# Kernel optimization log

Measured on AMD Instinct MI355X. Metric: run time of the kernel, lower is better.

## Reference

```python
import jax, jax.numpy as jnp
import numpy as np

N_NODES = 50000
N_EDGES = 800000
N_FEAT = 128
N_HID = 128
N_CLASS = 40


def _mean_aggregate(x, src, dst, num_nodes):
    # PyG 'mean' aggregation: for each target node, mean of source-neighbor features.
    msgs = x[src]                                             # [E, D] gather
    sums = jax.ops.segment_sum(msgs, dst, num_segments=num_nodes)   # [N, D]
    ones = jnp.ones((src.shape[0],), dtype=x.dtype)
    cnt = jax.ops.segment_sum(ones, dst, num_segments=num_nodes)    # [N]
    return sums / jnp.maximum(cnt, 1.0)[:, None]


def setup_inputs() -> dict:
    key = jax.random.key(0)
    ks = jax.random.split(key, 8)
    x = jax.random.normal(ks[0], (N_NODES, N_FEAT), dtype=jnp.float32)
    edge_index = jax.random.randint(ks[1], (2, N_EDGES), 0, N_NODES, dtype=jnp.int64)
    s1 = 1.0 / np.sqrt(N_FEAT)
    s2 = 1.0 / np.sqrt(N_HID)
    return {
        "x": x,
        "edge_index": edge_index,
        # SAGEConv 1: lin_l acts on aggregated neighbors (has bias), lin_r on root (no bias)
        "Wl1": jax.random.normal(ks[2], (N_FEAT, N_HID), dtype=jnp.float32) * s1,
        "Wr1": jax.random.normal(ks[3], (N_FEAT, N_HID), dtype=jnp.float32) * s1,
        "b1": jnp.zeros((N_HID,), dtype=jnp.float32),
        # SAGEConv 2 (gc2)
        "Wl2": jax.random.normal(ks[4], (N_HID, N_CLASS), dtype=jnp.float32) * s2,
        "Wr2": jax.random.normal(ks[5], (N_HID, N_CLASS), dtype=jnp.float32) * s2,
        "b2": jnp.zeros((N_CLASS,), dtype=jnp.float32),
    }


def reference(x, edge_index, Wl1, Wr1, b1, Wl2, Wr2, b2):
    src, dst = edge_index[0], edge_index[1]
    n = x.shape[0]
    # Layer 1: SAGEConv -> relu (dropout is identity in eval mode)
    agg = _mean_aggregate(x, src, dst, n)                 # [N, F]
    h = jax.nn.relu(agg @ Wl1 + x @ Wr1 + b1)             # [N, H]
    # Layer 2: SAGEConv (logits)
    agg2 = _mean_aggregate(h, src, dst, n)                # [N, H]
    out = agg2 @ Wl2 + h @ Wr2 + b2                       # [N, C]
    return out
```

## Files before the change

kernel.cpp:

```cpp
#include <hip/hip_runtime.h>
#include <hip/hip_bf16.h>

#define N_FEAT 128
#define N_HID  128
#define N_CLASS 40

#define NP   256
#define PSZ  196
#define BCAP 4096
#define BCHUNK 4096

#define HSTRIDE 136

typedef __attribute__((ext_vector_type(8))) __bf16 bf16x8;
typedef __attribute__((ext_vector_type(4))) float f32x4;

__device__ __forceinline__ unsigned short f2bf(float f) {
    union { float f; unsigned int u; } v; v.f = f;
    unsigned int r = (v.u + 0x7FFFu + ((v.u >> 16) & 1u)) >> 16;
    return (unsigned short)r;
}
__device__ __forceinline__ float bf2f_lo(unsigned int p) {
    union { unsigned int u; float f; } v; v.u = p << 16; return v.f;
}
__device__ __forceinline__ float bf2f_hi(unsigned int p) {
    union { unsigned int u; float f; } v; v.u = p & 0xFFFF0000u; return v.f;
}

__device__ __forceinline__ void swz_body(const float* __restrict__ W,
                                         unsigned short* __restrict__ sw,
                                         int ncols, int t, int nt) {
    if (t >= nt * 4 * 64) return;
    int lane = t & 63;
    int bi = t >> 6;
    int kc = bi & 3, ct = bi >> 2;
    int n = lane & 15, q = lane >> 4;
    int col = ct * 16 + n;
    #pragma unroll
    for (int j = 0; j < 8; ++j) {
        int k = kc * 32 + q * 8 + j;
        float f = (col < ncols) ? W[(size_t)k * ncols + col] : 0.f;
        sw[(size_t)t * 8 + j] = f2bf(f);
    }
}
__device__ __forceinline__ void swzc_body(const float* __restrict__ Wl2,
                                          const float* __restrict__ Wr2,
                                          unsigned short* __restrict__ sw, int t) {
    if (t >= 5 * 4 * 64) return;
    int lane = t & 63;
    int bi = t >> 6;
    int kc = bi & 3, ct = bi >> 2;
    int n = lane & 15, q = lane >> 4;
    int col = ct * 16 + n;
    #pragma unroll
    for (int j = 0; j < 8; ++j) {
        int k = kc * 32 + q * 8 + j;
        float f = (col < N_CLASS) ? Wl2[(size_t)k * N_CLASS + col]
                                  : Wr2[(size_t)k * N_CLASS + (col - N_CLASS)];
        sw[(size_t)t * 8 + j] = f2bf(f);
    }
}

__global__ __launch_bounds__(256) void k_prep(const float* __restrict__ x,
                                              unsigned short* __restrict__ xb, int nCvt, int nElem,
                                              const float* __restrict__ Wl1,
                                              const float* __restrict__ Wr1,
                                              const float* __restrict__ Wl2,
                                              const float* __restrict__ Wr2,
                                              unsigned short* __restrict__ w1l,
                                              unsigned short* __restrict__ w1r,
                                              unsigned short* __restrict__ wc,
                                              int* __restrict__ ptail) {
    int b = blockIdx.x, t = threadIdx.x;
    if (b < nCvt) {
        int i = (b * 256 + t) * 4;
        if (i < nElem) {
            float4 v = *(const float4*)(x + i);
            ushort4 o;
            o.x = f2bf(v.x); o.y = f2bf(v.y); o.z = f2bf(v.z); o.w = f2bf(v.w);
            *(ushort4*)(xb + i) = o;
        }
        return;
    }
    b -= nCvt;
    if (b < 8) { swz_body(Wl1, w1l, N_HID, b * 256 + t, 8); return; }
    b -= 8;
    if (b < 8) { swz_body(Wr1, w1r, N_HID, b * 256 + t, 8); return; }
    b -= 8;
    if (b < 5) { swzc_body(Wl2, Wr2, wc, b * 256 + t); return; }
    ptail[t] = 0;
}

__global__ __launch_bounds__(256) void k_bin(const int* __restrict__ src,
                                             const int* __restrict__ dst,
                                             int* __restrict__ ptail,
                                             uint2* __restrict__ bins, int E) {
    __shared__ uint2 stage[BCHUNK];
    __shared__ int lcnt[NP], lofs[NP], lcur[NP], gbase[NP];
    __shared__ int ws4[4];
    int t = threadIdx.x;
    int base = blockIdx.x * BCHUNK;
    int nE = min(BCHUNK, E - base);
    lcnt[t] = 0;
    __syncthreads();
    for (int i = t; i < nE; i += 256) {
        int d = dst[base + i];
        atomicAdd(&lcnt[d / PSZ], 1);
    }
    __syncthreads();
    {
        int v = lcnt[t];
        int lane = t & 63, wid = t >> 6;
        int inc = v;
        #pragma unroll
        for (int s = 1; s < 64; s <<= 1) {
            int u = __shfl_up(inc, s);
            if (lane >= s) inc += u;
        }
        if (lane == 63) ws4[wid] = inc;
        __syncthreads();
        int wb = 0;
        for (int w = 0; w < wid; ++w) wb += ws4[w];
        int exc = wb + inc - v;
        lofs[t] = exc;
        lcur[t] = exc;
        gbase[t] = atomicAdd(&ptail[t], v);
    }
    __syncthreads();
    for (int i = t; i < nE; i += 256) {
        int d = dst[base + i];
        int s = src[base + i];
        int pos = atomicAdd(&lcur[d / PSZ], 1);
        stage[pos] = make_uint2((unsigned)s, (unsigned)d);
    }
    __syncthreads();
    for (int i = t; i < nE; i += 256) {
        uint2 pr = stage[i];
        int p = (int)pr.y / PSZ;
        bins[(size_t)p * BCAP + gbase[p] + (i - lofs[p])] = pr;
    }
}

__global__ __launch_bounds__(256) void k_build(const uint2* __restrict__ bins,
                                               const int* __restrict__ ptail,
                                               int* __restrict__ off,
                                               int* __restrict__ srt, int N) {
    int p = blockIdx.x;
    int t = threadIdx.x;
    __shared__ int ws4[4];
    __shared__ int sexc[NP];
    __shared__ int lc[256], lofs[256];
    {
        int v = ptail[t];
        int lane = t & 63, wid = t >> 6;
        int inc = v;
        #pragma unroll
        for (int s = 1; s < 64; s <<= 1) {
            int u = __shfl_up(inc, s);
            if (lane >= s) inc += u;
        }
        if (lane == 63) ws4[wid] = inc;
        __syncthreads();
        int wb = 0;
        for (int w = 0; w < wid; ++w) wb += ws4[w];
        sexc[t] = wb + inc - v;
        if (p == NP - 1 && t == NP - 1) off[N] = wb + inc;
    }
    lc[t] = 0;
    __syncthreads();
    int pb = sexc[p];
    int n = ptail[p];
    const uint2* bp = bins + (size_t)p * BCAP;
    for (int i = t; i < n; i += 256)
        atomicAdd(&lc[(int)bp[i].y - p * PSZ], 1);
    __syncthreads();
    {
        int v = lc[t];
        int lane = t & 63, wid = t >> 6;
        int inc = v;
        #pragma unroll
        for (int s = 1; s < 64; s <<= 1) {
            int u = __shfl_up(inc, s);
            if (lane >= s) inc += u;
        }
        if (lane == 63) ws4[wid] = inc;
        __syncthreads();
        int wb = 0;
        for (int w = 0; w < wid; ++w) wb += ws4[w];
        lofs[t] = pb + wb + inc - v;
    }
    __syncthreads();
    int g = p * PSZ + t;
    if (t < PSZ && g < N) off[g] = lofs[t];
    __syncthreads();
    for (int i = t; i < n; i += 256) {
        uint2 pr = bp[i];
        int pos = atomicAdd(&lofs[(int)pr.y - p * PSZ], 1);
        srt[pos] = (int)pr.x;
    }
}

__global__ __launch_bounds__(256) void k_aggb4(const unsigned short* __restrict__ feat,
                                               const int* __restrict__ srt,
                                               const int* __restrict__ off,
                                               unsigned short* __restrict__ outp, int n_nodes) {
    int wave = (blockIdx.x * blockDim.x + threadIdx.x) >> 6;
    int lane = threadIdx.x & 63;
    if (wave >= n_nodes) return;
    int q = lane >> 4;
    int l = lane & 15;
    int beg = off[wave];
    int end = off[wave + 1];
    float a0 = 0.f, a1 = 0.f, a2 = 0.f, a3 = 0.f,
          a4 = 0.f, a5 = 0.f, a6 = 0.f, a7 = 0.f;
    int e = beg + q;
    #define ACCUM128(P) { \
        a0 += bf2f_lo(P.x); a1 += bf2f_hi(P.x); \
        a2 += bf2f_lo(P.y); a3 += bf2f_hi(P.y); \
        a4 += bf2f_lo(P.z); a5 += bf2f_hi(P.z); \
        a6 += bf2f_lo(P.w); a7 += bf2f_hi(P.w); }
    for (; e + 4 < end; e += 8) {
        int s0 = srt[e];
        int s1 = srt[e + 4];
        uint4 p0 = *(const uint4*)(feat + (size_t)s0 * N_FEAT + l * 8);
        uint4 p1 = *(const uint4*)(feat + (size_t)s1 * N_FEAT + l * 8);
        ACCUM128(p0)
        ACCUM128(p1)
    }
    if (e < end) {
        int s0 = srt[e];
        uint4 p0 = *(const uint4*)(feat + (size_t)s0 * N_FEAT + l * 8);
        ACCUM128(p0)
    }
    #undef ACCUM128
    #define RED(A) A += __shfl_xor(A, 16); A += __shfl_xor(A, 32);
    RED(a0) RED(a1) RED(a2) RED(a3) RED(a4) RED(a5) RED(a6) RED(a7)
    #undef RED
    if (q == 0) {
        int c = end - beg;
        float inv = 1.0f / (float)(c > 1 ? c : 1);
        uint4 o;
        o.x = ((unsigned int)f2bf(a1 * inv) << 16) | f2bf(a0 * inv);
        o.y = ((unsigned int)f2bf(a3 * inv) << 16) | f2bf(a2 * inv);
        o.z = ((unsigned int)f2bf(a5 * inv) << 16) | f2bf(a4 * inv);
        o.w = ((unsigned int)f2bf(a7 * inv) << 16) | f2bf(a6 * inv);
        *(uint4*)(outp + (size_t)wave * N_FEAT + l * 8) = o;
    }
}

__global__ __launch_bounds__(256) void k_gemm12(const unsigned short* __restrict__ aggb,
                                                const unsigned short* __restrict__ xb,
                                                const unsigned short* __restrict__ Bl,
                                                const unsigned short* __restrict__ Br,
                                                const float* __restrict__ bias1,
                                                const unsigned short* __restrict__ Bc,
                                                const float* __restrict__ bias2,
                                                unsigned short* __restrict__ p2b,
                                                float* __restrict__ r2, int n_nodes) {
    __shared__ unsigned short hlds[4][16 * HSTRIDE];
    int tid = threadIdx.x;
    int wv = tid >> 6;
    int wid = (blockIdx.x * 256 + tid) >> 6;
    int lane = tid & 63;
    int nb = wid * 16;
    if (nb >= n_nodes) return;
    int m = lane & 15, q = lane >> 4;
    size_t abase = (size_t)(nb + m) * N_FEAT + q * 8;
    bf16x8 Aa0 = *(const bf16x8*)(aggb + abase);
    bf16x8 Aa1 = *(const bf16x8*)(aggb + abase + 32);
    bf16x8 Aa2 = *(const bf16x8*)(aggb + abase + 64);
    bf16x8 Aa3 = *(const bf16x8*)(aggb + abase + 96);
    bf16x8 Ax0 = *(const bf16x8*)(xb + abase);
    bf16x8 Ax1 = *(const bf16x8*)(xb + abase + 32);
    bf16x8 Ax2 = *(const bf16x8*)(xb + abase + 64);
    bf16x8 Ax3 = *(const bf16x8*)(xb + abase + 96);
    const bf16x8* blp = (const bf16x8*)Bl + lane;
    const bf16x8* brp = (const bf16x8*)Br + lane;
    unsigned short* hl = hlds[wv];

    #pragma unroll
    for (int ct = 0; ct < 8; ++ct) {
        f32x4 acc = {0.f, 0.f, 0.f, 0.f};
        acc = __builtin_amdgcn_mfma_f32_16x16x32_bf16(Aa0, blp[(ct*4+0)*64], acc, 0,0,0);
        acc = __builtin_amdgcn_mfma_f32_16x16x32_bf16(Ax0, brp[(ct*4+0)*64], acc, 0,0,0);
        acc = __builtin_amdgcn_mfma_f32_16x16x32_bf16(Aa1, blp[(ct*4+1)*64], acc, 0,0,0);
        acc = __builtin_amdgcn_mfma_f32_16x16x32_bf16(Ax1, brp[(ct*4+1)*64], acc, 0,0,0);
        acc = __builtin_amdgcn_mfma_f32_16x16x32_bf16(Aa2, blp[(ct*4+2)*64], acc, 0,0,0);
        acc = __builtin_amdgcn_mfma_f32_16x16x32_bf16(Ax2, brp[(ct*4+2)*64], acc, 0,0,0);
        acc = __builtin_amdgcn_mfma_f32_16x16x32_bf16(Aa3, blp[(ct*4+3)*64], acc, 0,0,0);
        acc = __builtin_amdgcn_mfma_f32_16x16x32_bf16(Ax3, brp[(ct*4+3)*64], acc, 0,0,0);
        int col = ct * 16 + m;
        float bv = bias1[col];
        hl[(q*4 + 0) * HSTRIDE + col] = f2bf(fmaxf(acc.x + bv, 0.f));
        hl[(q*4 + 1) * HSTRIDE + col] = f2bf(fmaxf(acc.y + bv, 0.f));
        hl[(q*4 + 2) * HSTRIDE + col] = f2bf(fmaxf(acc.z + bv, 0.f));
        hl[(q*4 + 3) * HSTRIDE + col] = f2bf(fmaxf(acc.w + bv, 0.f));
    }
    bf16x8 H0 = *(const bf16x8*)(hl + m * HSTRIDE + q * 8);
    bf16x8 H1 = *(const bf16x8*)(hl + m * HSTRIDE + q * 8 + 32);
    bf16x8 H2 = *(const bf16x8*)(hl + m * HSTRIDE + q * 8 + 64);
    bf16x8 H3 = *(const bf16x8*)(hl + m * HSTRIDE + q * 8 + 96);
    const bf16x8* bcp = (const bf16x8*)Bc + lane;

    #pragma unroll
    for (int ct = 0; ct < 5; ++ct) {
        f32x4 acc = {0.f, 0.f, 0.f, 0.f};
        acc = __builtin_amdgcn_mfma_f32_16x16x32_bf16(H0, bcp[(ct*4+0)*64], acc, 0,0,0);
        acc = __builtin_amdgcn_mfma_f32_16x16x32_bf16(H1, bcp[(ct*4+1)*64], acc, 0,0,0);
        acc = __builtin_amdgcn_mfma_f32_16x16x32_bf16(H2, bcp[(ct*4+2)*64], acc, 0,0,0);
        acc = __builtin_amdgcn_mfma_f32_16x16x32_bf16(H3, bcp[(ct*4+3)*64], acc, 0,0,0);
        int col = ct * 16 + m;
        if (col < N_CLASS) {
            p2b[(size_t)(nb + q*4 + 0) * N_CLASS + col] = f2bf(acc.x);
            p2b[(size_t)(nb + q*4 + 1) * N_CLASS + col] = f2bf(acc.y);
            p2b[(size_t)(nb + q*4 + 2) * N_CLASS + col] = f2bf(acc.z);
            p2b[(size_t)(nb + q*4 + 3) * N_CLASS + col] = f2bf(acc.w);
        } else {
            int rc = col - N_CLASS;
            float bv = bias2[rc];
            r2[(size_t)(nb + q*4 + 0) * N_CLASS + rc] = acc.x + bv;
            r2[(size_t)(nb + q*4 + 1) * N_CLASS + rc] = acc.y + bv;
            r2[(size_t)(nb + q*4 + 2) * N_CLASS + rc] = acc.z + bv;
            r2[(size_t)(nb + q*4 + 3) * N_CLASS + rc] = acc.w + bv;
        }
    }
}

__global__ __launch_bounds__(256) void k_agg40(const unsigned short* __restrict__ p2b,
                                               const float* __restrict__ r2,
                                               const int* __restrict__ srt,
                                               const int* __restrict__ off,
                                               float* __restrict__ outp, int n_nodes) {
    int wave = (blockIdx.x * blockDim.x + threadIdx.x) >> 6;
    int lane = threadIdx.x & 63;
    if (wave >= n_nodes) return;
    int q = lane >> 4;
    int l = lane & 15;
    bool act = l < 10;
    int beg = off[wave];
    int end = off[wave + 1];
    float a0 = 0.f, a1 = 0.f, a2 = 0.f, a3 = 0.f;
    int e = beg + q;
    #define ACCUM40(P) { \
        a0 += bf2f_lo(P.x); a1 += bf2f_hi(P.x); \
        a2 += bf2f_lo(P.y); a3 += bf2f_hi(P.y); }
    for (; e + 4 < end; e += 8) {
        int s0 = srt[e];
        int s1 = srt[e + 4];
        if (act) {
            uint2 p0 = *(const uint2*)(p2b + (size_t)s0 * N_CLASS + l * 4);
            uint2 p1 = *(const uint2*)(p2b + (size_t)s1 * N_CLASS + l * 4);
            ACCUM40(p0)
            ACCUM40(p1)
        }
    }
    if (e < end && act) {
        int s0 = srt[e];
        uint2 p0 = *(const uint2*)(p2b + (size_t)s0 * N_CLASS + l * 4);
        ACCUM40(p0)
    }
    #undef ACCUM40
    #define RED(A) A += __shfl_xor(A, 16); A += __shfl_xor(A, 32);
    RED(a0) RED(a1) RED(a2) RED(a3)
    #undef RED
    if (lane < 10) {
        int c = end - beg;
        float inv = 1.0f / (float)(c > 1 ? c : 1);
        float4 rr = *(const float4*)(r2 + (size_t)wave * N_CLASS + lane * 4);
        float4 o;
        o.x = fmaf(a0, inv, rr.x);
        o.y = fmaf(a1, inv, rr.y);
        o.z = fmaf(a2, inv, rr.z);
        o.w = fmaf(a3, inv, rr.w);
        *(float4*)(outp + (size_t)wave * N_CLASS + lane * 4) = o;
    }
}

extern "C" void kernel_launch(void* const* d_in, const int* in_sizes, int n_in,
                              void* d_out, int out_size, void* d_ws, size_t ws_size,
                              hipStream_t stream) {
    const float* x   = (const float*)d_in[0];
    const int*   ei  = (const int*)d_in[1];
    const float* Wl1 = (const float*)d_in[2];
    const float* Wr1 = (const float*)d_in[3];
    const float* b1  = (const float*)d_in[4];
    const float* Wl2 = (const float*)d_in[5];
    const float* Wr2 = (const float*)d_in[6];
    const float* b2  = (const float*)d_in[7];
    float* out = (float*)d_out;

    const int N = in_sizes[0] / N_FEAT;
    const int E = in_sizes[1] / 2;
    const int* src = ei;
    const int* dst = ei + E;

    unsigned short* xb   = (unsigned short*)d_ws;
    unsigned short* aggb = xb + (size_t)N * N_FEAT;
    unsigned short* p2b  = aggb + (size_t)N * N_FEAT;
    float* r2 = (float*)(p2b + (size_t)N * N_CLASS);
    uint2* bins = (uint2*)p2b;
    unsigned short* w1l  = (unsigned short*)(r2 + (size_t)N * N_CLASS);
    unsigned short* w1r  = w1l + 16384;
    unsigned short* wc   = w1r + 16384;
    int* off = (int*)(wc + 10240);
    int* srt = off + N + 1;
    int* ptail = srt + E;

    const int TB = 256;
    int nCvt = (N * N_FEAT / 4 + TB - 1) / TB;
    int bblocks = (E + BCHUNK - 1) / BCHUNK;

    k_prep<<<nCvt + 8 + 8 + 5 + 1, TB, 0, stream>>>(x, xb, nCvt, N * N_FEAT,
                                                    Wl1, Wr1, Wl2, Wr2,
                                                    w1l, w1r, wc, ptail);
    k_bin<<<bblocks, TB, 0, stream>>>(src, dst, ptail, bins, E);
    k_build<<<NP, TB, 0, stream>>>(bins, ptail, off, srt, N);

    int aggblocks = (N * 64 + TB - 1) / TB;
    int gblocks = ((N + 15) / 16 + 3) / 4;

    k_aggb4<<<aggblocks, TB, 0, stream>>>(xb, srt, off, aggb, N);
    k_gemm12<<<gblocks, TB, 0, stream>>>(aggb, xb, w1l, w1r, b1, wc, b2, p2b, r2, N);
    k_agg40<<<aggblocks, TB, 0, stream>>>(p2b, r2, srt, off, out, N);
}
```

Baseline: 190.3 us.

## Fuse layer-1 neighbor aggregation into the GEMM kernel via LDS tile

Each wave now gathers and averages neighbor features for its 16 nodes directly into an LDS tile, then feeds that tile into the layer-1 and layer-2 projection MFMAs. This removes the separate aggregation kernel, its global bf16 intermediate write and reread, and one launch. In exchange, the gather runs serially over 16 nodes per wave, with far fewer waves in flight to hide memory latency.

New measurement: 224.8 us. +18.2%, slower.

```diff
diff --git a/kernel.cpp b/kernel.cpp
--- a/kernel.cpp
+++ b/kernel.cpp
@@ -200,83 +200,79 @@
     }
 }
 
-__global__ __launch_bounds__(256) void k_aggb4(const unsigned short* __restrict__ feat,
-                                               const int* __restrict__ srt,
-                                               const int* __restrict__ off,
-                                               unsigned short* __restrict__ outp, int n_nodes) {
-    int wave = (blockIdx.x * blockDim.x + threadIdx.x) >> 6;
-    int lane = threadIdx.x & 63;
-    if (wave >= n_nodes) return;
-    int q = lane >> 4;
-    int l = lane & 15;
-    int beg = off[wave];
-    int end = off[wave + 1];
-    float a0 = 0.f, a1 = 0.f, a2 = 0.f, a3 = 0.f,
-          a4 = 0.f, a5 = 0.f, a6 = 0.f, a7 = 0.f;
-    int e = beg + q;
-    #define ACCUM128(P) { \
-        a0 += bf2f_lo(P.x); a1 += bf2f_hi(P.x); \
-        a2 += bf2f_lo(P.y); a3 += bf2f_hi(P.y); \
-        a4 += bf2f_lo(P.z); a5 += bf2f_hi(P.z); \
-        a6 += bf2f_lo(P.w); a7 += bf2f_hi(P.w); }
-    for (; e + 4 < end; e += 8) {
-        int s0 = srt[e];
-        int s1 = srt[e + 4];
-        uint4 p0 = *(const uint4*)(feat + (size_t)s0 * N_FEAT + l * 8);
-        uint4 p1 = *(const uint4*)(feat + (size_t)s1 * N_FEAT + l * 8);
-        ACCUM128(p0)
-        ACCUM128(p1)
-    }
-    if (e < end) {
-        int s0 = srt[e];
-        uint4 p0 = *(const uint4*)(feat + (size_t)s0 * N_FEAT + l * 8);
-        ACCUM128(p0)
-    }
-    #undef ACCUM128
-    #define RED(A) A += __shfl_xor(A, 16); A += __shfl_xor(A, 32);
-    RED(a0) RED(a1) RED(a2) RED(a3) RED(a4) RED(a5) RED(a6) RED(a7)
-    #undef RED
-    if (q == 0) {
-        int c = end - beg;
-        float inv = 1.0f / (float)(c > 1 ? c : 1);
-        uint4 o;
-        o.x = ((unsigned int)f2bf(a1 * inv) << 16) | f2bf(a0 * inv);
-        o.y = ((unsigned int)f2bf(a3 * inv) << 16) | f2bf(a2 * inv);
-        o.z = ((unsigned int)f2bf(a5 * inv) << 16) | f2bf(a4 * inv);
-        o.w = ((unsigned int)f2bf(a7 * inv) << 16) | f2bf(a6 * inv);
-        *(uint4*)(outp + (size_t)wave * N_FEAT + l * 8) = o;
-    }
-}
-
-__global__ __launch_bounds__(256) void k_gemm12(const unsigned short* __restrict__ aggb,
-                                                const unsigned short* __restrict__ xb,
-                                                const unsigned short* __restrict__ Bl,
-                                                const unsigned short* __restrict__ Br,
-                                                const float* __restrict__ bias1,
-                                                const unsigned short* __restrict__ Bc,
-                                                const float* __restrict__ bias2,
-                                                unsigned short* __restrict__ p2b,
-                                                float* __restrict__ r2, int n_nodes) {
-    __shared__ unsigned short hlds[4][16 * HSTRIDE];
+__global__ __launch_bounds__(256) void k_fag(const unsigned short* __restrict__ xb,
+                                             const int* __restrict__ srt,
+                                             const int* __restrict__ off,
+                                             const unsigned short* __restrict__ Bl,
+                                             const unsigned short* __restrict__ Br,
+                                             const float* __restrict__ bias1,
+                                             const unsigned short* __restrict__ Bc,
+                                             const float* __restrict__ bias2,
+                                             unsigned short* __restrict__ p2b,
+                                             float* __restrict__ r2, int n_nodes) {
+    __shared__ unsigned short tile[4][16 * HSTRIDE];
     int tid = threadIdx.x;
     int wv = tid >> 6;
     int wid = (blockIdx.x * 256 + tid) >> 6;
     int lane = tid & 63;
     int nb = wid * 16;
     if (nb >= n_nodes) return;
-    int m = lane & 15, q = lane >> 4;
+    int q = lane >> 4;
+    int l = lane & 15;
+    unsigned short* tl = tile[wv];
+
+    for (int j = 0; j < 16; ++j) {
+        int beg = off[nb + j];
+        int end = off[nb + j + 1];
+        float a0 = 0.f, a1 = 0.f, a2 = 0.f, a3 = 0.f,
+              a4 = 0.f, a5 = 0.f, a6 = 0.f, a7 = 0.f;
+        int e = beg + q;
+        #define ACCUM128(P) { \
+            a0 += bf2f_lo(P.x); a1 += bf2f_hi(P.x); \
+            a2 += bf2f_lo(P.y); a3 += bf2f_hi(P.y); \
+            a4 += bf2f_lo(P.z); a5 += bf2f_hi(P.z); \
+            a6 += bf2f_lo(P.w); a7 += bf2f_hi(P.w); }
+        for (; e + 4 < end; e += 8) {
+            int s0 = srt[e];
+            int s1 = srt[e + 4];
+            uint4 p0 = *(const uint4*)(xb + (size_t)s0 * N_FEAT + l * 8);
+            uint4 p1 = *(const uint4*)(xb + (size_t)s1 * N_FEAT + l * 8);
+            ACCUM128(p0)
+            ACCUM128(p1)
+        }
+        if (e < end) {
+            int s0 = srt[e];
+            uint4 p0 = *(const uint4*)(xb + (size_t)s0 * N_FEAT + l * 8);
+            ACCUM128(p0)
+        }
+        #undef ACCUM128
+        #define RED(A) A += __shfl_xor(A, 16); A += __shfl_xor(A, 32);
+        RED(a0) RED(a1) RED(a2) RED(a3) RED(a4) RED(a5) RED(a6) RED(a7)
+        #undef RED
+        if (q == 0) {
+            int c = end - beg;
+            float inv = 1.0f / (float)(c > 1 ? c : 1);
+            uint4 o;
+            o.x = ((unsigned int)f2bf(a1 * inv) << 16) | f2bf(a0 * inv);
+            o.y = ((unsigned int)f2bf(a3 * inv) << 16) | f2bf(a2 * inv);
+            o.z = ((unsigned int)f2bf(a5 * inv) << 16) | f2bf(a4 * inv);
+            o.w = ((unsigned int)f2bf(a7 * inv) << 16) | f2bf(a6 * inv);
+            *(uint4*)(tl + j * HSTRIDE + l * 8) = o;
+        }
+    }
+
+    int m = l;
+    bf16x8 Aa0 = *(const bf16x8*)(tl + m * HSTRIDE + q * 8);
+    bf16x8 Aa1 = *(const bf16x8*)(tl + m * HSTRIDE + q * 8 + 32);
+    bf16x8 Aa2 = *(const bf16x8*)(tl + m * HSTRIDE + q * 8 + 64);
+    bf16x8 Aa3 = *(const bf16x8*)(tl + m * HSTRIDE + q * 8 + 96);
     size_t abase = (size_t)(nb + m) * N_FEAT + q * 8;
-    bf16x8 Aa0 = *(const bf16x8*)(aggb + abase);
-    bf16x8 Aa1 = *(const bf16x8*)(aggb + abase + 32);
-    bf16x8 Aa2 = *(const bf16x8*)(aggb + abase + 64);
-    bf16x8 Aa3 = *(const bf16x8*)(aggb + abase + 96);
     bf16x8 Ax0 = *(const bf16x8*)(xb + abase);
     bf16x8 Ax1 = *(const bf16x8*)(xb + abase + 32);
     bf16x8 Ax2 = *(const bf16x8*)(xb + abase + 64);
     bf16x8 Ax3 = *(const bf16x8*)(xb + abase + 96);
     const bf16x8* blp = (const bf16x8*)Bl + lane;
     const bf16x8* brp = (const bf16x8*)Br + lane;
-    unsigned short* hl = hlds[wv];
 
     #pragma unroll
     for (int ct = 0; ct < 8; ++ct) {
@@ -291,15 +287,15 @@
         acc = __builtin_amdgcn_mfma_f32_16x16x32_bf16(Ax3, brp[(ct*4+3)*64], acc, 0,0,0);
         int col = ct * 16 + m;
         float bv = bias1[col];
-        hl[(q*4 + 0) * HSTRIDE + col] = f2bf(fmaxf(acc.x + bv, 0.f));
-        hl[(q*4 + 1) * HSTRIDE + col] = f2bf(fmaxf(acc.y + bv, 0.f));
-        hl[(q*4 + 2) * HSTRIDE + col] = f2bf(fmaxf(acc.z + bv, 0.f));
-        hl[(q*4 + 3) * HSTRIDE + col] = f2bf(fmaxf(acc.w + bv, 0.f));
-    }
-    bf16x8 H0 = *(const bf16x8*)(hl + m * HSTRIDE + q * 8);
-    bf16x8 H1 = *(const bf16x8*)(hl + m * HSTRIDE + q * 8 + 32);
-    bf16x8 H2 = *(const bf16x8*)(hl + m * HSTRIDE + q * 8 + 64);
-    bf16x8 H3 = *(const bf16x8*)(hl + m * HSTRIDE + q * 8 + 96);
+        tl[(q*4 + 0) * HSTRIDE + col] = f2bf(fmaxf(acc.x + bv, 0.f));
+        tl[(q*4 + 1) * HSTRIDE + col] = f2bf(fmaxf(acc.y + bv, 0.f));
+        tl[(q*4 + 2) * HSTRIDE + col] = f2bf(fmaxf(acc.z + bv, 0.f));
+        tl[(q*4 + 3) * HSTRIDE + col] = f2bf(fmaxf(acc.w + bv, 0.f));
+    }
+    bf16x8 H0 = *(const bf16x8*)(tl + m * HSTRIDE + q * 8);
+    bf16x8 H1 = *(const bf16x8*)(tl + m * HSTRIDE + q * 8 + 32);
+    bf16x8 H2 = *(const bf16x8*)(tl + m * HSTRIDE + q * 8 + 64);
+    bf16x8 H3 = *(const bf16x8*)(tl + m * HSTRIDE + q * 8 + 96);
     const bf16x8* bcp = (const bf16x8*)Bc + lane;
 
     #pragma unroll
@@ -395,8 +391,7 @@
     const int* dst = ei + E;
 
     unsigned short* xb   = (unsigned short*)d_ws;
-    unsigned short* aggb = xb + (size_t)N * N_FEAT;
-    unsigned short* p2b  = aggb + (size_t)N * N_FEAT;
+    unsigned short* p2b  = xb + (size_t)N * N_FEAT;
     float* r2 = (float*)(p2b + (size_t)N * N_CLASS);
     uint2* bins = (uint2*)p2b;
     unsigned short* w1l  = (unsigned short*)(r2 + (size_t)N * N_CLASS);
@@ -419,7 +414,6 @@
     int aggblocks = (N * 64 + TB - 1) / TB;
     int gblocks = ((N + 15) / 16 + 3) / 4;
 
-    k_aggb4<<<aggblocks, TB, 0, stream>>>(xb, srt, off, aggb, N);
-    k_gemm12<<<gblocks, TB, 0, stream>>>(aggb, xb, w1l, w1r, b1, wc, b2, p2b, r2, N);
+    k_fag<<<gblocks, TB, 0, stream>>>(xb, srt, off, w1l, w1r, b1, wc, b2, p2b, r2, N);
     k_agg40<<<aggblocks, TB, 0, stream>>>(p2b, r2, srt, off, out, N);
 }
```
